# Kernel optimization log

Hardware: AMD Instinct MI355X
Metric: run time of the kernel (lower is better)

Reference implementation:

```python
import jax, jax.numpy as jnp
import numpy as np

N_CLASSES = 16
N_FEATURES = 64
BATCH = 4
TOP_K = 100
EMA_THETA = 0.9
TAU = 0.1
V = 262144  # 64^3 voxels, pre-flattened spatial dim


def setup_inputs() -> dict:
    key = jax.random.key(0)
    k1, k2, k3 = jax.random.split(key, 3)
    proba = jax.random.uniform(k1, (BATCH, N_CLASSES, V), dtype=jnp.float32)
    labels = jax.random.randint(k2, (BATCH, V), 0, N_CLASSES)
    # y must be one-hot: original uses torch.where(y > 0) and argmax(y, dim=1)
    y = jax.nn.one_hot(labels, N_CLASSES, axis=1, dtype=jnp.float32)  # [B,C,V]
    embeddings = jax.random.normal(k3, (BATCH, N_FEATURES, V), dtype=jnp.float32)
    return {"proba": proba, "y": y, "embeddings": embeddings}


def reference(proba, y, embeddings):
    B, C, _ = proba.shape
    Fd = embeddings.shape[1]
    K = TOP_K

    # --- update_average_class_representation (EMA from zero init):
    # avg[c] = 0*(1-theta) + theta*mean_rep[c] if class c present else 0
    mask = y > 0  # [B,C,V]
    count = mask.sum((0, 2))  # [C]
    sums = jnp.einsum('bcv,bfv->cf', mask.astype(embeddings.dtype), embeddings)
    mean_rep = sums / jnp.maximum(count, 1)[:, None].astype(embeddings.dtype)
    avg = jnp.where((count > 0)[:, None], EMA_THETA * mean_rep, 0.0)  # [C,F]

    # --- update_hard_examples: per-batch top-k on prod of probabilities
    labels = jnp.argmax(y, axis=1)  # [B,V]
    weights = jnp.prod(proba, axis=1)  # [B,V]
    _, idx = jax.lax.top_k(weights, K)  # [B,K]
    he = jnp.take_along_axis(embeddings, idx[:, None, :], axis=2).transpose(0, 2, 1)  # [B,K,F]
    hec = jnp.take_along_axis(labels, idx, axis=1)  # [B,K]

    # --- l_anco (vectorized over batch and class via masking):
    # num_i = exp(he_i * avg_c / tau); neg_den_j = sum_{c'!=c} exp(he_j * avg_c' / tau)
    # out[i,j,f] = log(num_i + neg_j) - log(num_i)  (torch broadcast [Nk,F] vs [Nk,1,F])
    logits = he[:, :, None, :] * avg[None, None, :, :] / TAU  # [B,K,C,F]
    E = jnp.exp(logits)  # [B,K,C,F]
    neg = E.sum(2, keepdims=True) - E  # [B,K,C,F] : sum over other classes
    pair = jnp.log(E[:, :, None] + neg[:, None]) - logits[:, :, None]  # [B,K,K,C,F]
    maskc = (hec[:, :, None] == jnp.arange(C)[None, None, :]).astype(pair.dtype)  # [B,K,C]
    num_sum = jnp.einsum('bijcf,bic,bjc->bc', pair, maskc, maskc)  # [B,C]
    nk = maskc.sum(1)  # [B,C] examples per (batch, class)
    denom = jnp.maximum(nk * nk * Fd, 1.0)
    output = jnp.where(nk > 0, num_sum / denom, 0.0)  # mean over [Nk,Nk,F]
    return -output.sum() / B
```

## Files before the change

### kernel.cpp

```cpp
#include <hip/hip_runtime.h>
#include <hip/hip_bf16.h>

#define V_ 262144
#define B_ 4
#define C_ 16
#define F_ 64
#define K_ 100
#define CAP_ 8192

#define OFF_WEIGHTS 0
#define OFF_LABELS  4194304
#define OFF_ZERO    5242880
#define OFF_HIST    5242880
#define OFF_CNT     5275648
#define OFF_SUMS    5275712
#define OFF_CCNT    5279808
#define ZERO_BYTES  36944
#define OFF_THRESH  5279824
#define OFF_CVAL    5279840
#define OFF_CIDX    5410912

__global__ __launch_bounds__(256) void k_stream(const float* __restrict__ proba,
                                                const float* __restrict__ y,
                                                float* __restrict__ weights,
                                                unsigned char* __restrict__ labels,
                                                int* __restrict__ hist,
                                                int* __restrict__ cnt)
{
    const int b = blockIdx.y;
    const int tid = threadIdx.x;
    const int q = blockIdx.x * 512 + tid;

    __shared__ int lhist[2048];
    __shared__ int lcnt[16];
    for (int i = tid; i < 2048; i += 256) lhist[i] = 0;
    if (tid < 16) lcnt[tid] = 0;
    __syncthreads();

    const float4* pb = (const float4*)(proba + ((size_t)b * C_) * V_) + q;
    const float4* yb = (const float4*)(y     + ((size_t)b * C_) * V_) + q;
    const int s4 = V_ >> 2;

    float4 p0 = pb[0], p1 = pb[256];
    int4 l0 = make_int4(0, 0, 0, 0);
    int4 l1 = make_int4(0, 0, 0, 0);

    #pragma unroll
    for (int c = 1; c < C_; c++) {
        float4 a0 = pb[c * s4], a1 = pb[c * s4 + 256];
        float4 q0 = yb[c * s4], q1 = yb[c * s4 + 256];
        p0.x *= a0.x; p0.y *= a0.y; p0.z *= a0.z; p0.w *= a0.w;
        p1.x *= a1.x; p1.y *= a1.y; p1.z *= a1.z; p1.w *= a1.w;
        if (q0.x > 0.f) l0.x = c;
        if (q0.y > 0.f) l0.y = c;
        if (q0.z > 0.f) l0.z = c;
        if (q0.w > 0.f) l0.w = c;
        if (q1.x > 0.f) l1.x = c;
        if (q1.y > 0.f) l1.y = c;
        if (q1.z > 0.f) l1.z = c;
        if (q1.w > 0.f) l1.w = c;
    }

    float4* wout = (float4*)(weights + (size_t)b * V_);
    wout[q] = p0; wout[q + 256] = p1;
    uchar4* lout = (uchar4*)(labels + (size_t)b * V_);
    lout[q]       = make_uchar4((unsigned char)l0.x, (unsigned char)l0.y,
                                (unsigned char)l0.z, (unsigned char)l0.w);
    lout[q + 256] = make_uchar4((unsigned char)l1.x, (unsigned char)l1.y,
                                (unsigned char)l1.z, (unsigned char)l1.w);

    float wv[8] = {p0.x, p0.y, p0.z, p0.w, p1.x, p1.y, p1.z, p1.w};
    int   lv[8] = {l0.x, l0.y, l0.z, l0.w, l1.x, l1.y, l1.z, l1.w};
    #pragma unroll
    for (int j = 0; j < 8; j++) {
        atomicAdd(&lcnt[lv[j]], 1);
        atomicAdd(&lhist[__float_as_uint(wv[j]) >> 21], 1);
    }
    __syncthreads();
    if (tid < 16) atomicAdd(&cnt[tid], lcnt[tid]);
    for (int i = tid; i < 2048; i += 256)
        if (lhist[i]) atomicAdd(&hist[b * 2048 + i], lhist[i]);
}

__global__ __launch_bounds__(512) void k_sums(const float* __restrict__ emb,
                                              const unsigned char* __restrict__ labels,
                                              float* __restrict__ sums)
{
    __shared__ float lacc[512 * 17];
    __shared__ float part[512];
    const int tid = threadIdx.x;

    const int id  = blockIdx.x;
    const int xcd = id & 7;
    const int grp = id >> 3;
    const int f   = (grp << 1) | (xcd & 1);
    const int b   = xcd >> 1;

    const float4* src = (const float4*)(emb + (((size_t)b << 6) + f) * V_);
    const unsigned int* lb = (const unsigned int*)(labels + (size_t)b * V_);

    float acc[16];
    #pragma unroll
    for (int c = 0; c < 16; c++) acc[c] = 0.f;

    for (int it = 0; it < 16; it++) {
        float4 v[8];
        unsigned lu[8];
        #pragma unroll
        for (int g = 0; g < 8; g++) {
            const int i4 = it * 4096 + g * 512 + tid;
            v[g]  = src[i4];
            lu[g] = lb[i4];
        }
        __builtin_amdgcn_sched_barrier(0);
        #pragma unroll
        for (int g = 0; g < 8; g++) {
            const int l0 =  lu[g]        & 0xff;
            const int l1 = (lu[g] >>  8) & 0xff;
            const int l2 = (lu[g] >> 16) & 0xff;
            const int l3 =  lu[g] >> 24;
            #pragma unroll
            for (int c = 0; c < 16; c++) {
                float s = (l0 == c ? v[g].x : 0.f);
                s      += (l1 == c ? v[g].y : 0.f);
                s      += (l2 == c ? v[g].z : 0.f);
                s      += (l3 == c ? v[g].w : 0.f);
                acc[c] += s;
            }
        }
    }

    #pragma unroll
    for (int c = 0; c < 16; c++) lacc[tid * 17 + c] = acc[c];
    __syncthreads();

    {
        const int c = tid & 15, r0 = (tid >> 4) << 4;
        float s = 0.f;
        #pragma unroll
        for (int i = 0; i < 16; i++) s += lacc[(r0 + i) * 17 + c];
        part[tid] = s;
    }
    __syncthreads();
    if (tid < 16) {
        float s = 0.f;
        #pragma unroll
        for (int j = 0; j < 32; j++) s += part[j * 16 + tid];
        atomicAdd(&sums[(tid << 6) + f], s);
    }
}

__global__ __launch_bounds__(256) void k_collect(const float* __restrict__ weights,
                                                 const int* __restrict__ hist,
                                                 int* __restrict__ ccnt,
                                                 float* __restrict__ cval,
                                                 int* __restrict__ cidx)
{
    const int b = blockIdx.y;
    const int tid = threadIdx.x;
    __shared__ int part[256];
    __shared__ int suf[257];
    __shared__ int sT;

    const int* h = hist + b * 2048;
    int loc[8]; int s = 0;
    #pragma unroll
    for (int i = 0; i < 8; i++) { loc[i] = h[tid * 8 + i]; s += loc[i]; }
    part[tid] = s;
    __syncthreads();
    if (tid == 0) {
        suf[256] = 0;
        for (int t = 255; t >= 0; t--) suf[t] = suf[t + 1] + part[t];
    }
    __syncthreads();
    int cg[9];
    cg[8] = suf[tid + 1];
    #pragma unroll
    for (int i = 7; i >= 0; i--) cg[i] = cg[i + 1] + loc[i];
    #pragma unroll
    for (int i = 0; i < 8; i++)
        if (cg[i] >= K_ && cg[i + 1] < K_) sT = tid * 8 + i;
    __syncthreads();

    const unsigned T = (unsigned)sT;
    const int v = (blockIdx.x * 256 + tid) * 4;
    float4 w = *(const float4*)(weights + (size_t)b * V_ + v);
    float wv[4] = {w.x, w.y, w.z, w.w};
    for (int j = 0; j < 4; j++) {
        unsigned bits = __float_as_uint(wv[j]);
        if ((bits >> 21) >= T) {
            int p = atomicAdd(&ccnt[b], 1);
            if (p < CAP_) {
                cval[b * CAP_ + p] = wv[j];
                cidx[b * CAP_ + p] = v + j;
            }
        }
    }
}

__global__ __launch_bounds__(256) void k_final(const float* __restrict__ emb,
                                               const unsigned char* __restrict__ labels,
                                               const float* __restrict__ sums,
                                               const int* __restrict__ cnt,
                                               const int* __restrict__ ccnt,
                                               const float* __restrict__ cval,
                                               const int* __restrict__ cidx,
                                               float* __restrict__ out)
{
    const int b = blockIdx.x, tid = threadIdx.x;
    __shared__ float avg[1024];
    __shared__ float ec[K_ * 64];
    __shared__ float Ssum[K_ * 64];
    __shared__ float lsum[K_];
    __shared__ int selIdx[K_];
    __shared__ int selLab[K_];
    __shared__ int nk[16];
    __shared__ int lists[16 * K_];
    __shared__ int ofs[17];
    __shared__ float red[256];

    for (int i = tid; i < 1024; i += 256) {
        int c = i >> 6;
        float cn = (float)cnt[c];
        avg[i] = (cn > 0.f) ? 0.9f * sums[i] / fmaxf(cn, 1.f) : 0.f;
    }
    if (tid < K_) { lsum[tid] = 0.f; selIdx[tid] = 0; }
    if (tid < 16) nk[tid] = 0;

    int M = ccnt[b]; if (M > CAP_) M = CAP_;
    const float* cv = cval + b * CAP_;
    const int*   ci = cidx + b * CAP_;
    for (int i = tid; i < M; i += 256) {
        float v = cv[i]; int id = ci[i];
        int rank = 0;
        for (int j = 0; j < M; j++) {
            float vj = cv[j];
            rank += (vj > v) || (vj == v && ci[j] < id);
        }
        if (rank < K_) selIdx[rank] = id;
    }
    __syncthreads();
    for (int i = tid; i < K_; i += 256) selLab[i] = labels[(size_t)b * V_ + selIdx[i]];
    __syncthreads();
    if (tid == 0) {
        for (int i = 0; i < K_; i++) { int c = selLab[i]; lists[c * K_ + nk[c]] = i; nk[c]++; }
        int o = 0;
        for (int c = 0; c < 16; c++) { ofs[c] = o; o += nk[c] * nk[c]; }
        ofs[16] = o;
    }
    __syncthreads();

    for (int e = tid; e < K_ * 64; e += 256) {
        int k = e >> 6, f = e & 63;
        float h = emb[(((size_t)b << 6) + f) * V_ + selIdx[k]];
        int lab = selLab[k];
        float s = 0.f, ev = 0.f, lvv = 0.f;
        for (int c = 0; c < 16; c++) {
            float l = h * avg[(c << 6) + f] / 0.1f;
            float x = expf(l);
            s += x;
            if (c == lab) { ev = x; lvv = l; }
        }
        ec[e] = ev; Ssum[e] = s;
        atomicAdd(&lsum[k], lvv);
    }
    __syncthreads();

    const int P = ofs[16];
    float accv = 0.f;
    for (int p = tid; p < P; p += 256) {
        int c = 0;
        while (p >= ofs[c + 1]) c++;
        int loc = p - ofs[c];
        int n = nk[c];
        int i = lists[c * K_ + loc / n];
        int j = lists[c * K_ + loc % n];
        const float* eci = &ec[i << 6];
        const float* ecj = &ec[j << 6];
        const float* sj  = &Ssum[j << 6];
        float s = 0.f;
        for (int f = 0; f < 64; f++) s += logf(eci[f] + sj[f] - ecj[f]);
        accv += s / ((float)n * (float)n * 64.f);
    }
    for (int i2 = tid; i2 < K_; i2 += 256) {
        int c = selLab[i2];
        accv -= lsum[i2] / ((float)nk[c] * 64.f);
    }
    red[tid] = accv;
    __syncthreads();
    for (int s2 = 128; s2 > 0; s2 >>= 1) {
        if (tid < s2) red[tid] += red[tid + s2];
        __syncthreads();
    }
    if (tid == 0) atomicAdd(out, -red[0] / (float)B_);
}

extern "C" void kernel_launch(void* const* d_in, const int* in_sizes, int n_in,
                              void* d_out, int out_size, void* d_ws, size_t ws_size,
                              hipStream_t stream) {
    const float* proba = (const float*)d_in[0];
    const float* y     = (const float*)d_in[1];
    const float* emb   = (const float*)d_in[2];
    char* ws = (char*)d_ws;

    float* weights        = (float*)(ws + OFF_WEIGHTS);
    unsigned char* labels = (unsigned char*)(ws + OFF_LABELS);
    int* hist             = (int*)(ws + OFF_HIST);
    int* cnt              = (int*)(ws + OFF_CNT);
    float* sums           = (float*)(ws + OFF_SUMS);
    int* ccnt             = (int*)(ws + OFF_CCNT);
    float* cval           = (float*)(ws + OFF_CVAL);
    int* cidx             = (int*)(ws + OFF_CIDX);
    float* out            = (float*)d_out;

    hipMemsetAsync(ws + OFF_ZERO, 0, ZERO_BYTES, stream);
    hipMemsetAsync(out, 0, sizeof(float), stream);

    k_stream<<<dim3(V_ / 2048, B_), 256, 0, stream>>>(proba, y, weights, labels, hist, cnt);
    k_sums<<<256, 512, 0, stream>>>(emb, labels, sums);
    k_collect<<<dim3(V_ / 1024, B_), 256, 0, stream>>>(weights, hist, ccnt, cval, cidx);
    k_final<<<B_, 256, 0, stream>>>(emb, labels, sums, cnt, ccnt, cval, cidx, out);
}
```

Measured before the change: 533.6 us.

## Share label tile in LDS across eight features per block in k_sums

Each k_sums block used to handle one (batch, feature) pair and read the whole label stream from global memory. Now each block takes a V/8 segment and stages its labels once in shared memory, and each of its eight wavefronts processes a different feature against that tile. This is meant to cut redundant global label reads by eight times. The block reduction is rearranged to give per-wave results, which means more atomics and 32KB of extra LDS per block. The XCD-aware block mapping is also dropped.

```diff
diff --git a/kernel.cpp b/kernel.cpp
--- a/kernel.cpp
+++ b/kernel.cpp
@@ -86,18 +86,30 @@
                                               const unsigned char* __restrict__ labels,
                                               float* __restrict__ sums)
 {
+    __shared__ unsigned int slab[8192];
     __shared__ float lacc[512 * 17];
     __shared__ float part[512];
-    const int tid = threadIdx.x;
-
-    const int id  = blockIdx.x;
-    const int xcd = id & 7;
-    const int grp = id >> 3;
-    const int f   = (grp << 1) | (xcd & 1);
-    const int b   = xcd >> 1;
-
-    const float4* src = (const float4*)(emb + (((size_t)b << 6) + f) * V_);
-    const unsigned int* lb = (const unsigned int*)(labels + (size_t)b * V_);
+    const int tid  = threadIdx.x;
+    const int lane = tid & 63;
+    const int sg   = tid >> 6;
+
+    const int seg = blockIdx.x;
+    const int fg  = blockIdx.y;
+    const int b   = blockIdx.z;
+    const int f   = (fg << 3) + sg;
+    const int vlen = V_ / 8;
+
+    {
+        const uint4* lg = (const uint4*)(labels + (size_t)b * V_ + (size_t)seg * vlen);
+        uint4* sl4 = (uint4*)slab;
+        #pragma unroll
+        for (int i = 0; i < 4; i++)
+            sl4[i * 512 + tid] = lg[i * 512 + tid];
+    }
+    __syncthreads();
+
+    const float4* src = (const float4*)(emb + (((size_t)b << 6) + f) * V_
+                                        + (size_t)seg * vlen);
 
     float acc[16];
     #pragma unroll
@@ -108,9 +120,9 @@
         unsigned lu[8];
         #pragma unroll
         for (int g = 0; g < 8; g++) {
-            const int i4 = it * 4096 + g * 512 + tid;
+            const int i4 = it * 512 + g * 64 + lane;
             v[g]  = src[i4];
-            lu[g] = lb[i4];
+            lu[g] = slab[i4];
         }
         __builtin_amdgcn_sched_barrier(0);
         #pragma unroll
@@ -133,20 +145,23 @@
     #pragma unroll
     for (int c = 0; c < 16; c++) lacc[tid * 17 + c] = acc[c];
     __syncthreads();
-
     {
-        const int c = tid & 15, r0 = (tid >> 4) << 4;
+        const int c    = tid & 15;
+        const int rgrp = (tid >> 4) & 3;
+        const int sgg  = tid >> 6;
         float s = 0.f;
         #pragma unroll
-        for (int i = 0; i < 16; i++) s += lacc[(r0 + i) * 17 + c];
+        for (int i = 0; i < 16; i++)
+            s += lacc[((sgg << 6) + (rgrp << 4) + i) * 17 + c];
         part[tid] = s;
     }
     __syncthreads();
-    if (tid < 16) {
-        float s = 0.f;
-        #pragma unroll
-        for (int j = 0; j < 32; j++) s += part[j * 16 + tid];
-        atomicAdd(&sums[(tid << 6) + f], s);
+    if ((tid & 48) == 0) {
+        const int c   = tid & 15;
+        const int sgg = tid >> 6;
+        float s = part[(sgg << 6) + c]      + part[(sgg << 6) + 16 + c]
+                + part[(sgg << 6) + 32 + c] + part[(sgg << 6) + 48 + c];
+        atomicAdd(&sums[(c << 6) + (fg << 3) + sgg], s);
     }
 }
 
@@ -317,7 +332,7 @@
     hipMemsetAsync(out, 0, sizeof(float), stream);
 
     k_stream<<<dim3(V_ / 2048, B_), 256, 0, stream>>>(proba, y, weights, labels, hist, cnt);
-    k_sums<<<256, 512, 0, stream>>>(emb, labels, sums);
+    k_sums<<<dim3(8, 8, B_), 512, 0, stream>>>(emb, labels, sums);
     k_collect<<<dim3(V_ / 1024, B_), 256, 0, stream>>>(weights, hist, ccnt, cval, cidx);
     k_final<<<B_, 256, 0, stream>>>(emb, labels, sums, cnt, ccnt, cval, cidx, out);
 }
```

Result: slower. 550.7 us (+3.2%).
